# Kernel optimization log

Hardware: AMD Instinct MI355X
Metric: run time of the kernel (lower is better)

## Reference

```python
import jax, jax.numpy as jnp
import numpy as np

N_NODES = 100000
N_EDGES = 1000000
IN_F = 64
HEADS = 4
OUT_C = 32  # per-head channels
EDGE_DIM = 16
NEG_SLOPE = 0.2


def setup_inputs() -> dict:
    key = jax.random.key(0)
    ks = jax.random.split(key, 10)
    x = jax.random.normal(ks[0], (N_NODES, IN_F), dtype=jnp.float32)
    edge_index = jax.random.randint(ks[1], (2, N_EDGES), 0, N_NODES, dtype=jnp.int64)
    edge_attr = jax.random.normal(ks[2], (N_EDGES, EDGE_DIM), dtype=jnp.float32)
    s = 1.0 / np.sqrt(IN_F)
    W = jax.random.normal(ks[3], (IN_F, HEADS * OUT_C), dtype=jnp.float32) * s
    W_edge = jax.random.normal(ks[4], (EDGE_DIM, HEADS * OUT_C), dtype=jnp.float32) * (1.0 / np.sqrt(EDGE_DIM))
    att_src = jax.random.normal(ks[5], (HEADS, OUT_C), dtype=jnp.float32) * (1.0 / np.sqrt(OUT_C))
    att_dst = jax.random.normal(ks[6], (HEADS, OUT_C), dtype=jnp.float32) * (1.0 / np.sqrt(OUT_C))
    att_edge = jax.random.normal(ks[7], (HEADS, OUT_C), dtype=jnp.float32) * (1.0 / np.sqrt(OUT_C))
    bias = jnp.zeros((HEADS * OUT_C,), dtype=jnp.float32)
    return {"x": x, "edge_index": edge_index, "edge_attr": edge_attr,
            "W": W, "W_edge": W_edge, "att_src": att_src, "att_dst": att_dst,
            "att_edge": att_edge, "bias": bias}


def reference(x, edge_index, edge_attr, W, W_edge, att_src, att_dst, att_edge, bias):
    # PyG GATConv with edge_dim, add_self_loops=False, concat=True.
    N = x.shape[0]
    src = edge_index[0]  # message source j
    dst = edge_index[1]  # message target i

    x_proj = (x @ W).reshape(N, HEADS, OUT_C)          # [N,H,C]
    a_src = jnp.einsum('nhc,hc->nh', x_proj, att_src)  # [N,H]
    a_dst = jnp.einsum('nhc,hc->nh', x_proj, att_dst)  # [N,H]

    e_proj = (edge_attr @ W_edge).reshape(-1, HEADS, OUT_C)  # [E,H,C]
    a_edge = jnp.einsum('ehc,hc->eh', e_proj, att_edge)      # [E,H]

    alpha = a_src[src] + a_dst[dst] + a_edge                 # [E,H]
    alpha = jax.nn.leaky_relu(alpha, NEG_SLOPE)

    # edge softmax grouped by destination node
    seg_max = jax.ops.segment_max(alpha, dst, num_segments=N)  # [N,H]
    alpha = jnp.exp(alpha - seg_max[dst])
    denom = jax.ops.segment_sum(alpha, dst, num_segments=N)    # [N,H]
    alpha = alpha / (denom[dst] + 1e-16)

    msg = x_proj[src] * alpha[:, :, None]                      # [E,H,C]
    out = jax.ops.segment_sum(msg, dst, num_segments=N)        # [N,H,C]
    return out.reshape(N, HEADS * OUT_C) + bias
```

## Files before the change

### kernel.cpp

```cpp
#include <hip/hip_runtime.h>
#include <hip/hip_fp16.h>


#define HC 128
#define NEG 0.2f
#define CH 16
#define K_SHIFT 6.0f
#define NBK 512
#define BSH 8
#define BMSK 255
#define BCAP 3584
#define EPB 2048

typedef __fp16 half2_t __attribute__((ext_vector_type(2)));

__device__ __forceinline__ unsigned short f2bf(float f) {
    unsigned u = __float_as_uint(f);
    return (unsigned short)((u + 0x7fffu + ((u >> 16) & 1u)) >> 16);
}
__device__ __forceinline__ unsigned pk_h2(float lo, float hi) {
    half2_t p = __builtin_amdgcn_cvt_pkrtz(lo, hi);
    union { half2_t h; unsigned u; } cv;
    cv.h = p;
    return cv.u;
}
__device__ __forceinline__ float h2f_bits(unsigned short bits) {
    __half_raw hr; hr.x = bits;
    return __half2float(*reinterpret_cast<__half*>(&hr));
}
__device__ __forceinline__ long ld_idx(const int* __restrict__ ei, long i, int m64) {
    return m64 ? (long)(((const long long*)ei)[i]) : (long)ei[i];
}
__device__ __forceinline__ int detect_m64(const int* __restrict__ ei, int* s_m64) {
    int t = threadIdx.x;
    if (t < 64) {
        unsigned long long bal = __ballot(ei[2 * t + 1] != 0);
        if (t == 0) *s_m64 = (bal == 0ull) ? 1 : 0;
    }
    __syncthreads();
    return *s_m64;
}

union FrontLDS {
    struct {
        int hist[NBK]; int gb[NBK]; int loff[NBK]; int cnt2[NBK]; int s_sc[NBK];
        unsigned sd_l[EPB];
        unsigned short bk_l[EPB];
        uint2 aev_l[EPB];
    } b;
    struct {
        float x_s[4][64][68];
    } p;
};

__global__ __launch_bounds__(1024) void k_front(
    const float* __restrict__ x, const float* __restrict__ W,
    const float* __restrict__ as_, const float* __restrict__ ad_,
    const float* __restrict__ We, const float* __restrict__ ae,
    const float* __restrict__ eattr, const int* __restrict__ ei,
    unsigned short* __restrict__ xp, float* __restrict__ a_src,
    float* __restrict__ a_dst, int* __restrict__ bcur,
    unsigned* __restrict__ sdstg, uint2* __restrict__ aevstg,
    int N, int E, int nbA, int nbP) {
    __shared__ FrontLDS L;
    __shared__ float q_s[64];
    __shared__ int s_m64;
    int t = threadIdx.x;
    int id = blockIdx.x;

    bool bucket_role;
    int rid;
    if (id < 2 * nbP) { bucket_role = !(id & 1); rid = id >> 1; }
    else              { bucket_role = true;      rid = nbP + (id - 2 * nbP); }

    if (bucket_role) {
        int m64 = detect_m64(ei, &s_m64);
        if (t < 64) {
            int dd = t >> 2, h = t & 3;
            float s = 0.f;
            for (int c = 0; c < 32; ++c)
                s += We[dd * HC + h * 32 + c] * ae[h * 32 + c];
            q_s[t] = s;
        }
        if (t < NBK) { L.b.hist[t] = 0; L.b.cnt2[t] = 0; }
        __syncthreads();

        int base = rid * EPB + t;
#pragma unroll
        for (int k = 0; k < 2; ++k) {
            int e = base + k * 1024;
            if (e < E) {
                int d = (int)ld_idx(ei, (long)E + e, m64);
                atomicAdd(&L.b.hist[d >> BSH], 1);
            }
        }
        __syncthreads();
        if (t < NBK) {
            int c = L.b.hist[t];
            L.b.gb[t] = c ? atomicAdd(&bcur[t], c) : 0;
        }
        int own = (t < NBK) ? L.b.hist[t] : 0;
        if (t < NBK) L.b.s_sc[t] = own;
        __syncthreads();
        for (int off = 1; off < NBK; off <<= 1) {
            int xv = (t < NBK && t >= off) ? L.b.s_sc[t - off] : 0;
            __syncthreads();
            if (t < NBK) L.b.s_sc[t] += xv;
            __syncthreads();
        }
        if (t < NBK) L.b.loff[t] = L.b.s_sc[t] - own;
        __syncthreads();

#pragma unroll
        for (int k = 0; k < 2; ++k) {
            int e = base + k * 1024;
            if (e >= E) continue;
            int d = (int)ld_idx(ei, (long)E + e, m64);
            int b = d >> BSH;
            int lr = atomicAdd(&L.b.cnt2[b], 1);
            long s = ld_idx(ei, e, m64);
            const float4* pe = reinterpret_cast<const float4*>(eattr + (long)e * 16);
            float4 e0 = pe[0], e1 = pe[1], e2 = pe[2], e3 = pe[3];
            float ev[16] = {e0.x, e0.y, e0.z, e0.w, e1.x, e1.y, e1.z, e1.w,
                            e2.x, e2.y, e2.z, e2.w, e3.x, e3.y, e3.z, e3.w};
            float ov[4];
#pragma unroll
            for (int h = 0; h < 4; ++h) {
                float aev = 0.f;
#pragma unroll
                for (int dd = 0; dd < 16; ++dd) aev += ev[dd] * q_s[dd * 4 + h];
                ov[h] = aev;
            }
            int li = L.b.loff[b] + lr;
            L.b.sd_l[li] = (unsigned)s | ((unsigned)(d & BMSK) << 20);
            L.b.bk_l[li] = (unsigned short)b;
            L.b.aev_l[li] = make_uint2(pk_h2(ov[0], ov[1]), pk_h2(ov[2], ov[3]));
        }
        __syncthreads();

        int nrec = E - rid * EPB;
        if (nrec > EPB) nrec = EPB;
#pragma unroll
        for (int k = 0; k < 2; ++k) {
            int i = k * 1024 + t;
            if (i >= nrec) continue;
            int b = L.b.bk_l[i];
            int off = L.b.gb[b] + (i - L.b.loff[b]);
            if (off >= BCAP) continue;
            sdstg[b * BCAP + off] = L.b.sd_l[i];
            aevstg[b * BCAP + off] = L.b.aev_l[i];
        }
        return;
    }

    int q = t >> 8, tid = t & 255;
    int n0 = rid * 256 + q * 64;
    float (*x_s)[68] = L.p.x_s[q];
#pragma unroll
    for (int i = 0; i < 4; ++i) {
        int fl = i * 256 + tid;
        int node = fl >> 4, f4 = fl & 15;
        float4 v = make_float4(0.f, 0.f, 0.f, 0.f);
        if (n0 + node < N)
            v = *reinterpret_cast<const float4*>(&x[(long)(n0 + node) * 64 + f4 * 4]);
        x_s[f4 * 4 + 0][node] = v.x;
        x_s[f4 * 4 + 1][node] = v.y;
        x_s[f4 * 4 + 2][node] = v.z;
        x_s[f4 * 4 + 3][node] = v.w;
    }
    __syncthreads();

    int c = tid & 31;
    int nd = tid >> 5;
    const float4* __restrict__ W4 = reinterpret_cast<const float4*>(W);
    float acc[8][4];
#pragma unroll
    for (int i = 0; i < 8; ++i)
#pragma unroll
        for (int j = 0; j < 4; ++j) acc[i][j] = 0.f;

#pragma unroll 8
    for (int k = 0; k < 64; ++k) {
        float4 w4 = W4[k * 32 + c];
        float4 xa = *reinterpret_cast<const float4*>(&x_s[k][nd * 8]);
        float4 xb = *reinterpret_cast<const float4*>(&x_s[k][nd * 8 + 4]);
        float xv[8] = {xa.x, xa.y, xa.z, xa.w, xb.x, xb.y, xb.z, xb.w};
#pragma unroll
        for (int i = 0; i < 8; ++i) {
            acc[i][0] += xv[i] * w4.x;
            acc[i][1] += xv[i] * w4.y;
            acc[i][2] += xv[i] * w4.z;
            acc[i][3] += xv[i] * w4.w;
        }
    }

    float4 s4 = *reinterpret_cast<const float4*>(&as_[c * 4]);
    float4 d4 = *reinterpret_cast<const float4*>(&ad_[c * 4]);
#pragma unroll
    for (int i = 0; i < 8; ++i) {
        int node = n0 + nd * 8 + i;
        if (node < N) {
            ushort4 o;
            o.x = f2bf(acc[i][0]); o.y = f2bf(acc[i][1]);
            o.z = f2bf(acc[i][2]); o.w = f2bf(acc[i][3]);
            *reinterpret_cast<ushort4*>(&xp[(long)node * HC + c * 4]) = o;
        }
        float ps = acc[i][0] * s4.x + acc[i][1] * s4.y + acc[i][2] * s4.z + acc[i][3] * s4.w;
        float pd = acc[i][0] * d4.x + acc[i][1] * d4.y + acc[i][2] * d4.z + acc[i][3] * d4.w;
#pragma unroll
        for (int off = 1; off < 8; off <<= 1) {
            ps += __shfl_xor(ps, off, 64);
            pd += __shfl_xor(pd, off, 64);
        }
        if ((c & 7) == 0 && node < N) {
            int h = c >> 3;
            a_src[(long)node * 4 + h] = ps;
            a_dst[(long)node * 4 + h] = pd;
        }
    }
}

__global__ __launch_bounds__(1024) void k_back(
    const unsigned* __restrict__ sdstg, const uint2* __restrict__ aevstg,
    const int* __restrict__ bcur, const float* __restrict__ a_src,
    const float* __restrict__ a_dst, const char* __restrict__ xpc,
    const float* __restrict__ bias, float* __restrict__ out, int N) {
    int b = blockIdx.x, t = threadIdx.x;
    __shared__ int deg_l[256];
    __shared__ int s_sc[256];
    __shared__ int pfx[256];
    __shared__ unsigned src_l[BCAP];
    __shared__ uint2 w_l[BCAP];
    __shared__ float s_ex[16][CH][4];
    __shared__ int s_off[16][CH];
    __shared__ float s_l[16][4];
    if (t < 256) deg_l[t] = 0;
    __syncthreads();
    int cnt = bcur[b]; if (cnt > BCAP) cnt = BCAP;

    unsigned sdr[4]; int rkr[4]; uint2 wr[4];
#pragma unroll
    for (int k = 0; k < 4; ++k) {
        int i = k * 1024 + t;
        sdr[k] = 0u; rkr[k] = -1; wr[k] = make_uint2(0u, 0u);
        if (i < cnt) {
            unsigned sd = sdstg[b * BCAP + i];
            sdr[k] = sd;
            int dl = (sd >> 20) & BMSK;
            rkr[k] = atomicAdd(&deg_l[dl], 1);
            int s = (int)(sd & 0xFFFFFu);
            uint2 av = aevstg[b * BCAP + i];
            float4 s4 = *reinterpret_cast<const float4*>(a_src + (long)s * 4);
            float4 d4 = *reinterpret_cast<const float4*>(a_dst + (long)(b * 256 + dl) * 4);
            float lf[4];
            lf[0] = s4.x + d4.x + h2f_bits((unsigned short)(av.x & 0xffffu));
            lf[1] = s4.y + d4.y + h2f_bits((unsigned short)(av.x >> 16));
            lf[2] = s4.z + d4.z + h2f_bits((unsigned short)(av.y & 0xffffu));
            lf[3] = s4.w + d4.w + h2f_bits((unsigned short)(av.y >> 16));
            float exv[4];
#pragma unroll
            for (int h = 0; h < 4; ++h) {
                float v = (lf[h] > 0.f) ? lf[h] : NEG * lf[h];
                exv[h] = __expf(v - K_SHIFT);
            }
            wr[k] = make_uint2(pk_h2(exv[0], exv[1]), pk_h2(exv[2], exv[3]));
        }
    }
    __syncthreads();
    int own = (t < 256) ? deg_l[t] : 0;
    if (t < 256) s_sc[t] = own;
    __syncthreads();
    for (int off = 1; off < 256; off <<= 1) {
        int xv = (t >= off && t < 256) ? s_sc[t - off] : 0;
        __syncthreads();
        if (t < 256) s_sc[t] += xv;
        __syncthreads();
    }
    if (t < 256) pfx[t] = s_sc[t] - own;
    __syncthreads();
#pragma unroll
    for (int k = 0; k < 4; ++k) {
        int i = k * 1024 + t;
        if (i >= cnt) continue;
        int dl = (sdr[k] >> 20) & BMSK;
        int pos = pfx[dl] + rkr[k];
        src_l[pos] = sdr[k] & 0xFFFFFu;
        w_l[pos] = wr[k];
    }
    __syncthreads();

    int wv = t >> 6, lane = t & 63;
    int h_s = lane & 3, e_s = lane >> 2;
    int par = lane >> 5;
    int cl = lane & 31;
    int h_a = cl >> 3;
    for (int ni = 0; ni < 16; ++ni) {
        int dl = wv * 16 + ni;
        int n = b * 256 + dl;
        if (n >= N) continue;
        int beg = pfx[dl];
        int end = beg + deg_l[dl];
        if (end > BCAP) end = BCAP;
        float l = 0.f;
        float acc[4] = {0.f, 0.f, 0.f, 0.f};
        for (int cs = beg; cs < end; cs += CH) {
            int c2 = end - cs;
            if (c2 > CH) c2 = CH;
            float ex = 0.f;
            if (e_s < c2) {
                if (h_s == 0) s_off[wv][e_s] = (int)(src_l[cs + e_s] << 8);
                uint2 wv2 = w_l[cs + e_s];
                unsigned pr = (h_s & 2) ? wv2.y : wv2.x;
                unsigned bits = (h_s & 1) ? (pr >> 16) : (pr & 0xffffu);
                ex = h2f_bits((unsigned short)bits);
            }
            s_ex[wv][e_s][h_s] = ex;
            float se = ex;
            se += __shfl_xor(se, 4, 64);
            se += __shfl_xor(se, 8, 64);
            se += __shfl_xor(se, 16, 64);
            se += __shfl_xor(se, 32, 64);
            l += se;
            int j = 0;
            for (; j + 4 <= c2; j += 4) {
                int ea0 = j + par, ea1 = j + 2 + par;
                int o0 = s_off[wv][ea0], o1 = s_off[wv][ea1];
                float w0 = s_ex[wv][ea0][h_a], w1 = s_ex[wv][ea1][h_a];
                uint2 v0 = *reinterpret_cast<const uint2*>(xpc + o0 + cl * 8);
                uint2 v1 = *reinterpret_cast<const uint2*>(xpc + o1 + cl * 8);
                acc[0] += w0 * __uint_as_float(v0.x << 16);
                acc[1] += w0 * __uint_as_float(v0.x & 0xffff0000u);
                acc[2] += w0 * __uint_as_float(v0.y << 16);
                acc[3] += w0 * __uint_as_float(v0.y & 0xffff0000u);
                acc[0] += w1 * __uint_as_float(v1.x << 16);
                acc[1] += w1 * __uint_as_float(v1.x & 0xffff0000u);
                acc[2] += w1 * __uint_as_float(v1.y << 16);
                acc[3] += w1 * __uint_as_float(v1.y & 0xffff0000u);
            }
            for (; j < c2; j += 2) {
                int e = j + par;
                bool act = e < c2;
                int o = s_off[wv][act ? e : j];
                float w = act ? s_ex[wv][e][h_a] : 0.f;
                uint2 v = *reinterpret_cast<const uint2*>(xpc + o + cl * 8);
                acc[0] += w * __uint_as_float(v.x << 16);
                acc[1] += w * __uint_as_float(v.x & 0xffff0000u);
                acc[2] += w * __uint_as_float(v.y << 16);
                acc[3] += w * __uint_as_float(v.y & 0xffff0000u);
            }
        }
        if (lane < 4) s_l[wv][h_s] = l;
#pragma unroll
        for (int k = 0; k < 4; ++k) acc[k] += __shfl_xor(acc[k], 32, 64);
        if (par == 0) {
            float d = s_l[wv][h_a] + 1e-16f;
            float4 b4 = *reinterpret_cast<const float4*>(bias + cl * 4);
            float4 o;
            o.x = acc[0] / d + b4.x;
            o.y = acc[1] / d + b4.y;
            o.z = acc[2] / d + b4.z;
            o.w = acc[3] / d + b4.w;
            *reinterpret_cast<float4*>(out + (long)n * HC + cl * 4) = o;
        }
    }
}

extern "C" void kernel_launch(void* const* d_in, const int* in_sizes, int n_in,
                              void* d_out, int out_size, void* d_ws, size_t ws_size,
                              hipStream_t stream) {
    const float* x    = (const float*)d_in[0];
    const int*   ei   = (const int*)d_in[1];
    const float* ea   = (const float*)d_in[2];
    const float* W    = (const float*)d_in[3];
    const float* We   = (const float*)d_in[4];
    const float* as_  = (const float*)d_in[5];
    const float* ad_  = (const float*)d_in[6];
    const float* ae   = (const float*)d_in[7];
    const float* bias = (const float*)d_in[8];
    float* out = (float*)d_out;

    int N = in_sizes[0] / 64;
    int E = in_sizes[1] / 2;

    char* ws = (char*)d_ws;
    size_t off = 0;
    auto take = [&](size_t bytes) -> char* {
        char* p = ws + off;
        off += (bytes + 511) & ~(size_t)511;
        return p;
    };
    unsigned short* xp = (unsigned short*)take((size_t)N * HC * 2);
    float* a_src    = (float*)take((size_t)N * 4 * 4);
    float* a_dst    = (float*)take((size_t)N * 4 * 4);
    unsigned* sdstg = (unsigned*)take((size_t)NBK * BCAP * 4);
    uint2* aevstg   = (uint2*)take((size_t)NBK * BCAP * 8);
    int* bcur       = (int*)take((size_t)NBK * 4);

    int nbA = (E + EPB - 1) / EPB;
    int nbP = (N + 255) / 256;

    (void)hipMemsetAsync(bcur, 0, (size_t)NBK * 4, stream);
    hipLaunchKernelGGL(k_front, dim3(nbA + nbP), dim3(1024), 0, stream,
                       x, W, as_, ad_, We, ae, ea, ei,
                       xp, a_src, a_dst, bcur, sdstg, aevstg, N, E, nbA, nbP);
    hipLaunchKernelGGL(k_back, dim3(nbP), dim3(1024), 0, stream,
                       sdstg, aevstg, bcur, a_src, a_dst,
                       (const char*)xp, bias, out, N);
}
```

Baseline: 245.7 us.

## Merge front and back kernels into one persistent cooperative kernel with grid sync

Fuses the projection/bucketing kernel and the aggregation kernel into a single persistent cooperative kernel. Blocks loop over front work items, meet at a grid-wide barrier, then loop over destination buckets. The goal is to remove the second kernel launch and its inter-kernel gap. In exchange, the grid is capped at occupancy times 256 CUs, and the shared LDS union grows to the larger back-phase footprint, which may lower occupancy of the front phase.

```diff
diff --git a/kernel.cpp b/kernel.cpp
--- a/kernel.cpp
+++ b/kernel.cpp
@@ -1,5 +1,8 @@
 #include <hip/hip_runtime.h>
 #include <hip/hip_fp16.h>
+#include <hip/hip_cooperative_groups.h>
+
+namespace cg = cooperative_groups;
 
 
 #define HC 128
@@ -41,7 +44,7 @@
     return *s_m64;
 }
 
-union FrontLDS {
+union AllLDS {
     struct {
         int hist[NBK]; int gb[NBK]; int loff[NBK]; int cnt2[NBK]; int s_sc[NBK];
         unsigned sd_l[EPB];
@@ -51,9 +54,17 @@
     struct {
         float x_s[4][64][68];
     } p;
+    struct {
+        int deg_l[256]; int s_sc[256]; int pfx[256];
+        unsigned src_l[BCAP];
+        uint2 w_l[BCAP];
+        float s_ex[16][CH][4];
+        int s_off[16][CH];
+        float s_l[16][4];
+    } k;
 };
 
-__global__ __launch_bounds__(1024) void k_front(
+__global__ __launch_bounds__(1024) void k_all(
     const float* __restrict__ x, const float* __restrict__ W,
     const float* __restrict__ as_, const float* __restrict__ ad_,
     const float* __restrict__ We, const float* __restrict__ ae,
@@ -61,306 +72,303 @@
     unsigned short* __restrict__ xp, float* __restrict__ a_src,
     float* __restrict__ a_dst, int* __restrict__ bcur,
     unsigned* __restrict__ sdstg, uint2* __restrict__ aevstg,
+    const float* __restrict__ bias, float* __restrict__ out,
     int N, int E, int nbA, int nbP) {
-    __shared__ FrontLDS L;
+    __shared__ AllLDS L;
     __shared__ float q_s[64];
     __shared__ int s_m64;
     int t = threadIdx.x;
-    int id = blockIdx.x;
-
-    bool bucket_role;
-    int rid;
-    if (id < 2 * nbP) { bucket_role = !(id & 1); rid = id >> 1; }
-    else              { bucket_role = true;      rid = nbP + (id - 2 * nbP); }
-
-    if (bucket_role) {
-        int m64 = detect_m64(ei, &s_m64);
-        if (t < 64) {
-            int dd = t >> 2, h = t & 3;
-            float s = 0.f;
-            for (int c = 0; c < 32; ++c)
-                s += We[dd * HC + h * 32 + c] * ae[h * 32 + c];
-            q_s[t] = s;
-        }
-        if (t < NBK) { L.b.hist[t] = 0; L.b.cnt2[t] = 0; }
-        __syncthreads();
-
-        int base = rid * EPB + t;
-#pragma unroll
-        for (int k = 0; k < 2; ++k) {
-            int e = base + k * 1024;
-            if (e < E) {
+
+    int nFront = nbA + nbP;
+    int nMin = (nbA < nbP) ? nbA : nbP;
+    int nPair = 2 * nMin;
+    for (int item = blockIdx.x; item < nFront; item += gridDim.x) {
+        __syncthreads();
+        bool bucket_role; int rid;
+        if (item < nPair) { bucket_role = !(item & 1); rid = item >> 1; }
+        else              { bucket_role = (nbA > nbP); rid = nMin + (item - nPair); }
+
+        if (bucket_role) {
+            int m64 = detect_m64(ei, &s_m64);
+            if (t < 64) {
+                int dd = t >> 2, h = t & 3;
+                float s = 0.f;
+                for (int c = 0; c < 32; ++c)
+                    s += We[dd * HC + h * 32 + c] * ae[h * 32 + c];
+                q_s[t] = s;
+            }
+            if (t < NBK) { L.b.hist[t] = 0; L.b.cnt2[t] = 0; }
+            __syncthreads();
+
+            int base = rid * EPB + t;
+#pragma unroll
+            for (int k = 0; k < 2; ++k) {
+                int e = base + k * 1024;
+                if (e < E) {
+                    int d = (int)ld_idx(ei, (long)E + e, m64);
+                    atomicAdd(&L.b.hist[d >> BSH], 1);
+                }
+            }
+            __syncthreads();
+            if (t < NBK) {
+                int c = L.b.hist[t];
+                L.b.gb[t] = c ? atomicAdd(&bcur[t], c) : 0;
+            }
+            int own = (t < NBK) ? L.b.hist[t] : 0;
+            if (t < NBK) L.b.s_sc[t] = own;
+            __syncthreads();
+            for (int off = 1; off < NBK; off <<= 1) {
+                int xv = (t < NBK && t >= off) ? L.b.s_sc[t - off] : 0;
+                __syncthreads();
+                if (t < NBK) L.b.s_sc[t] += xv;
+                __syncthreads();
+            }
+            if (t < NBK) L.b.loff[t] = L.b.s_sc[t] - own;
+            __syncthreads();
+
+#pragma unroll
+            for (int k = 0; k < 2; ++k) {
+                int e = base + k * 1024;
+                if (e >= E) continue;
                 int d = (int)ld_idx(ei, (long)E + e, m64);
-                atomicAdd(&L.b.hist[d >> BSH], 1);
-            }
-        }
-        __syncthreads();
-        if (t < NBK) {
-            int c = L.b.hist[t];
-            L.b.gb[t] = c ? atomicAdd(&bcur[t], c) : 0;
-        }
-        int own = (t < NBK) ? L.b.hist[t] : 0;
-        if (t < NBK) L.b.s_sc[t] = own;
-        __syncthreads();
-        for (int off = 1; off < NBK; off <<= 1) {
-            int xv = (t < NBK && t >= off) ? L.b.s_sc[t - off] : 0;
-            __syncthreads();
-            if (t < NBK) L.b.s_sc[t] += xv;
-            __syncthreads();
-        }
-        if (t < NBK) L.b.loff[t] = L.b.s_sc[t] - own;
-        __syncthreads();
-
-#pragma unroll
-        for (int k = 0; k < 2; ++k) {
-            int e = base + k * 1024;
-            if (e >= E) continue;
-            int d = (int)ld_idx(ei, (long)E + e, m64);
-            int b = d >> BSH;
-            int lr = atomicAdd(&L.b.cnt2[b], 1);
-            long s = ld_idx(ei, e, m64);
-            const float4* pe = reinterpret_cast<const float4*>(eattr + (long)e * 16);
-            float4 e0 = pe[0], e1 = pe[1], e2 = pe[2], e3 = pe[3];
-            float ev[16] = {e0.x, e0.y, e0.z, e0.w, e1.x, e1.y, e1.z, e1.w,
-                            e2.x, e2.y, e2.z, e2.w, e3.x, e3.y, e3.z, e3.w};
-            float ov[4];
-#pragma unroll
-            for (int h = 0; h < 4; ++h) {
-                float aev = 0.f;
-#pragma unroll
-                for (int dd = 0; dd < 16; ++dd) aev += ev[dd] * q_s[dd * 4 + h];
-                ov[h] = aev;
-            }
-            int li = L.b.loff[b] + lr;
-            L.b.sd_l[li] = (unsigned)s | ((unsigned)(d & BMSK) << 20);
-            L.b.bk_l[li] = (unsigned short)b;
-            L.b.aev_l[li] = make_uint2(pk_h2(ov[0], ov[1]), pk_h2(ov[2], ov[3]));
-        }
-        __syncthreads();
-
-        int nrec = E - rid * EPB;
-        if (nrec > EPB) nrec = EPB;
-#pragma unroll
-        for (int k = 0; k < 2; ++k) {
-            int i = k * 1024 + t;
-            if (i >= nrec) continue;
-            int b = L.b.bk_l[i];
-            int off = L.b.gb[b] + (i - L.b.loff[b]);
-            if (off >= BCAP) continue;
-            sdstg[b * BCAP + off] = L.b.sd_l[i];
-            aevstg[b * BCAP + off] = L.b.aev_l[i];
-        }
-        return;
-    }
-
-    int q = t >> 8, tid = t & 255;
-    int n0 = rid * 256 + q * 64;
-    float (*x_s)[68] = L.p.x_s[q];
-#pragma unroll
-    for (int i = 0; i < 4; ++i) {
-        int fl = i * 256 + tid;
-        int node = fl >> 4, f4 = fl & 15;
-        float4 v = make_float4(0.f, 0.f, 0.f, 0.f);
-        if (n0 + node < N)
-            v = *reinterpret_cast<const float4*>(&x[(long)(n0 + node) * 64 + f4 * 4]);
-        x_s[f4 * 4 + 0][node] = v.x;
-        x_s[f4 * 4 + 1][node] = v.y;
-        x_s[f4 * 4 + 2][node] = v.z;
-        x_s[f4 * 4 + 3][node] = v.w;
-    }
-    __syncthreads();
-
-    int c = tid & 31;
-    int nd = tid >> 5;
-    const float4* __restrict__ W4 = reinterpret_cast<const float4*>(W);
-    float acc[8][4];
-#pragma unroll
-    for (int i = 0; i < 8; ++i)
-#pragma unroll
-        for (int j = 0; j < 4; ++j) acc[i][j] = 0.f;
+                int b = d >> BSH;
+                int lr = atomicAdd(&L.b.cnt2[b], 1);
+                long s = ld_idx(ei, e, m64);
+                const float4* pe = reinterpret_cast<const float4*>(eattr + (long)e * 16);
+                float4 e0 = pe[0], e1 = pe[1], e2 = pe[2], e3 = pe[3];
+                float ev[16] = {e0.x, e0.y, e0.z, e0.w, e1.x, e1.y, e1.z, e1.w,
+                                e2.x, e2.y, e2.z, e2.w, e3.x, e3.y, e3.z, e3.w};
+                float ov[4];
+#pragma unroll
+                for (int h = 0; h < 4; ++h) {
+                    float aev = 0.f;
+#pragma unroll
+                    for (int dd = 0; dd < 16; ++dd) aev += ev[dd] * q_s[dd * 4 + h];
+                    ov[h] = aev;
+                }
+                int li = L.b.loff[b] + lr;
+                L.b.sd_l[li] = (unsigned)s | ((unsigned)(d & BMSK) << 20);
+                L.b.bk_l[li] = (unsigned short)b;
+                L.b.aev_l[li] = make_uint2(pk_h2(ov[0], ov[1]), pk_h2(ov[2], ov[3]));
+            }
+            __syncthreads();
+
+            int nrec = E - rid * EPB;
+            if (nrec > EPB) nrec = EPB;
+#pragma unroll
+            for (int k = 0; k < 2; ++k) {
+                int i = k * 1024 + t;
+                if (i >= nrec) continue;
+                int b = L.b.bk_l[i];
+                int off = L.b.gb[b] + (i - L.b.loff[b]);
+                if (off >= BCAP) continue;
+                sdstg[b * BCAP + off] = L.b.sd_l[i];
+                aevstg[b * BCAP + off] = L.b.aev_l[i];
+            }
+        } else {
+            int q = t >> 8, tid = t & 255;
+            int n0 = rid * 256 + q * 64;
+            float (*x_s)[68] = L.p.x_s[q];
+#pragma unroll
+            for (int i = 0; i < 4; ++i) {
+                int fl = i * 256 + tid;
+                int node = fl >> 4, f4 = fl & 15;
+                float4 v = make_float4(0.f, 0.f, 0.f, 0.f);
+                if (n0 + node < N)
+                    v = *reinterpret_cast<const float4*>(&x[(long)(n0 + node) * 64 + f4 * 4]);
+                x_s[f4 * 4 + 0][node] = v.x;
+                x_s[f4 * 4 + 1][node] = v.y;
+                x_s[f4 * 4 + 2][node] = v.z;
+                x_s[f4 * 4 + 3][node] = v.w;
+            }
+            __syncthreads();
+
+            int c = tid & 31;
+            int nd = tid >> 5;
+            const float4* __restrict__ W4 = reinterpret_cast<const float4*>(W);
+            float acc[8][4];
+#pragma unroll
+            for (int i = 0; i < 8; ++i)
+#pragma unroll
+                for (int j = 0; j < 4; ++j) acc[i][j] = 0.f;
 
 #pragma unroll 8
-    for (int k = 0; k < 64; ++k) {
-        float4 w4 = W4[k * 32 + c];
-        float4 xa = *reinterpret_cast<const float4*>(&x_s[k][nd * 8]);
-        float4 xb = *reinterpret_cast<const float4*>(&x_s[k][nd * 8 + 4]);
-        float xv[8] = {xa.x, xa.y, xa.z, xa.w, xb.x, xb.y, xb.z, xb.w};
-#pragma unroll
-        for (int i = 0; i < 8; ++i) {
-            acc[i][0] += xv[i] * w4.x;
-            acc[i][1] += xv[i] * w4.y;
-            acc[i][2] += xv[i] * w4.z;
-            acc[i][3] += xv[i] * w4.w;
+            for (int k = 0; k < 64; ++k) {
+                float4 w4 = W4[k * 32 + c];
+                float4 xa = *reinterpret_cast<const float4*>(&x_s[k][nd * 8]);
+                float4 xb = *reinterpret_cast<const float4*>(&x_s[k][nd * 8 + 4]);
+                float xv[8] = {xa.x, xa.y, xa.z, xa.w, xb.x, xb.y, xb.z, xb.w};
+#pragma unroll
+                for (int i = 0; i < 8; ++i) {
+                    acc[i][0] += xv[i] * w4.x;
+                    acc[i][1] += xv[i] * w4.y;
+                    acc[i][2] += xv[i] * w4.z;
+                    acc[i][3] += xv[i] * w4.w;
+                }
+            }
+
+            float4 s4 = *reinterpret_cast<const float4*>(&as_[c * 4]);
+            float4 d4 = *reinterpret_cast<const float4*>(&ad_[c * 4]);
+#pragma unroll
+            for (int i = 0; i < 8; ++i) {
+                int node = n0 + nd * 8 + i;
+                if (node < N) {
+                    ushort4 o;
+                    o.x = f2bf(acc[i][0]); o.y = f2bf(acc[i][1]);
+                    o.z = f2bf(acc[i][2]); o.w = f2bf(acc[i][3]);
+                    *reinterpret_cast<ushort4*>(&xp[(long)node * HC + c * 4]) = o;
+                }
+                float ps = acc[i][0] * s4.x + acc[i][1] * s4.y + acc[i][2] * s4.z + acc[i][3] * s4.w;
+                float pd = acc[i][0] * d4.x + acc[i][1] * d4.y + acc[i][2] * d4.z + acc[i][3] * d4.w;
+#pragma unroll
+                for (int off = 1; off < 8; off <<= 1) {
+                    ps += __shfl_xor(ps, off, 64);
+                    pd += __shfl_xor(pd, off, 64);
+                }
+                if ((c & 7) == 0 && node < N) {
+                    int h = c >> 3;
+                    a_src[(long)node * 4 + h] = ps;
+                    a_dst[(long)node * 4 + h] = pd;
+                }
+            }
         }
     }
 
-    float4 s4 = *reinterpret_cast<const float4*>(&as_[c * 4]);
-    float4 d4 = *reinterpret_cast<const float4*>(&ad_[c * 4]);
-#pragma unroll
-    for (int i = 0; i < 8; ++i) {
-        int node = n0 + nd * 8 + i;
-        if (node < N) {
-            ushort4 o;
-            o.x = f2bf(acc[i][0]); o.y = f2bf(acc[i][1]);
-            o.z = f2bf(acc[i][2]); o.w = f2bf(acc[i][3]);
-            *reinterpret_cast<ushort4*>(&xp[(long)node * HC + c * 4]) = o;
+    __threadfence();
+    cg::this_grid().sync();
+    __threadfence();
+
+    for (int b = blockIdx.x; b < nbP; b += gridDim.x) {
+        __syncthreads();
+        if (t < 256) L.k.deg_l[t] = 0;
+        __syncthreads();
+        int cnt = bcur[b]; if (cnt > BCAP) cnt = BCAP;
+
+        unsigned sdr[4]; int rkr[4]; uint2 wr[4];
+#pragma unroll
+        for (int k = 0; k < 4; ++k) {
+            int i = k * 1024 + t;
+            sdr[k] = 0u; rkr[k] = -1; wr[k] = make_uint2(0u, 0u);
+            if (i < cnt) {
+                unsigned sd = sdstg[b * BCAP + i];
+                sdr[k] = sd;
+                int dl = (sd >> 20) & BMSK;
+                rkr[k] = atomicAdd(&L.k.deg_l[dl], 1);
+                int s = (int)(sd & 0xFFFFFu);
+                uint2 av = aevstg[b * BCAP + i];
+                float4 s4 = *reinterpret_cast<const float4*>(a_src + (long)s * 4);
+                float4 d4 = *reinterpret_cast<const float4*>(a_dst + (long)(b * 256 + dl) * 4);
+                float lf[4];
+                lf[0] = s4.x + d4.x + h2f_bits((unsigned short)(av.x & 0xffffu));
+                lf[1] = s4.y + d4.y + h2f_bits((unsigned short)(av.x >> 16));
+                lf[2] = s4.z + d4.z + h2f_bits((unsigned short)(av.y & 0xffffu));
+                lf[3] = s4.w + d4.w + h2f_bits((unsigned short)(av.y >> 16));
+                float exv[4];
+#pragma unroll
+                for (int h = 0; h < 4; ++h) {
+                    float v = (lf[h] > 0.f) ? lf[h] : NEG * lf[h];
+                    exv[h] = __expf(v - K_SHIFT);
+                }
+                wr[k] = make_uint2(pk_h2(exv[0], exv[1]), pk_h2(exv[2], exv[3]));
+            }
         }
-        float ps = acc[i][0] * s4.x + acc[i][1] * s4.y + acc[i][2] * s4.z + acc[i][3] * s4.w;
-        float pd = acc[i][0] * d4.x + acc[i][1] * d4.y + acc[i][2] * d4.z + acc[i][3] * d4.w;
-#pragma unroll
-        for (int off = 1; off < 8; off <<= 1) {
-            ps += __shfl_xor(ps, off, 64);
-            pd += __shfl_xor(pd, off, 64);
+        __syncthreads();
+        int own = (t < 256) ? L.k.deg_l[t] : 0;
+        if (t < 256) L.k.s_sc[t] = own;
+        __syncthreads();
+        for (int off = 1; off < 256; off <<= 1) {
+            int xv = (t >= off && t < 256) ? L.k.s_sc[t - off] : 0;
+            __syncthreads();
+            if (t < 256) L.k.s_sc[t] += xv;
+            __syncthreads();
         }
-        if ((c & 7) == 0 && node < N) {
-            int h = c >> 3;
-            a_src[(long)node * 4 + h] = ps;
-            a_dst[(long)node * 4 + h] = pd;
+        if (t < 256) L.k.pfx[t] = L.k.s_sc[t] - own;
+        __syncthreads();
+#pragma unroll
+        for (int k = 0; k < 4; ++k) {
+            int i = k * 1024 + t;
+            if (i >= cnt) continue;
+            int dl = (sdr[k] >> 20) & BMSK;
+            int pos = L.k.pfx[dl] + rkr[k];
+            L.k.src_l[pos] = sdr[k] & 0xFFFFFu;
+            L.k.w_l[pos] = wr[k];
         }
-    }
-}
-
-__global__ __launch_bounds__(1024) void k_back(
-    const unsigned* __restrict__ sdstg, const uint2* __restrict__ aevstg,
-    const int* __restrict__ bcur, const float* __restrict__ a_src,
-    const float* __restrict__ a_dst, const char* __restrict__ xpc,
-    const float* __restrict__ bias, float* __restrict__ out, int N) {
-    int b = blockIdx.x, t = threadIdx.x;
-    __shared__ int deg_l[256];
-    __shared__ int s_sc[256];
-    __shared__ int pfx[256];
-    __shared__ unsigned src_l[BCAP];
-    __shared__ uint2 w_l[BCAP];
-    __shared__ float s_ex[16][CH][4];
-    __shared__ int s_off[16][CH];
-    __shared__ float s_l[16][4];
-    if (t < 256) deg_l[t] = 0;
-    __syncthreads();
-    int cnt = bcur[b]; if (cnt > BCAP) cnt = BCAP;
-
-    unsigned sdr[4]; int rkr[4]; uint2 wr[4];
-#pragma unroll
-    for (int k = 0; k < 4; ++k) {
-        int i = k * 1024 + t;
-        sdr[k] = 0u; rkr[k] = -1; wr[k] = make_uint2(0u, 0u);
-        if (i < cnt) {
-            unsigned sd = sdstg[b * BCAP + i];
-            sdr[k] = sd;
-            int dl = (sd >> 20) & BMSK;
-            rkr[k] = atomicAdd(&deg_l[dl], 1);
-            int s = (int)(sd & 0xFFFFFu);
-            uint2 av = aevstg[b * BCAP + i];
-            float4 s4 = *reinterpret_cast<const float4*>(a_src + (long)s * 4);
-            float4 d4 = *reinterpret_cast<const float4*>(a_dst + (long)(b * 256 + dl) * 4);
-            float lf[4];
-            lf[0] = s4.x + d4.x + h2f_bits((unsigned short)(av.x & 0xffffu));
-            lf[1] = s4.y + d4.y + h2f_bits((unsigned short)(av.x >> 16));
-            lf[2] = s4.z + d4.z + h2f_bits((unsigned short)(av.y & 0xffffu));
-            lf[3] = s4.w + d4.w + h2f_bits((unsigned short)(av.y >> 16));
-            float exv[4];
-#pragma unroll
-            for (int h = 0; h < 4; ++h) {
-                float v = (lf[h] > 0.f) ? lf[h] : NEG * lf[h];
-                exv[h] = __expf(v - K_SHIFT);
-            }
-            wr[k] = make_uint2(pk_h2(exv[0], exv[1]), pk_h2(exv[2], exv[3]));
-        }
-    }
-    __syncthreads();
-    int own = (t < 256) ? deg_l[t] : 0;
-    if (t < 256) s_sc[t] = own;
-    __syncthreads();
-    for (int off = 1; off < 256; off <<= 1) {
-        int xv = (t >= off && t < 256) ? s_sc[t - off] : 0;
-        __syncthreads();
-        if (t < 256) s_sc[t] += xv;
-        __syncthreads();
-    }
-    if (t < 256) pfx[t] = s_sc[t] - own;
-    __syncthreads();
-#pragma unroll
-    for (int k = 0; k < 4; ++k) {
-        int i = k * 1024 + t;
-        if (i >= cnt) continue;
-        int dl = (sdr[k] >> 20) & BMSK;
-        int pos = pfx[dl] + rkr[k];
-        src_l[pos] = sdr[k] & 0xFFFFFu;
-        w_l[pos] = wr[k];
-    }
-    __syncthreads();
-
-    int wv = t >> 6, lane = t & 63;
-    int h_s = lane & 3, e_s = lane >> 2;
-    int par = lane >> 5;
-    int cl = lane & 31;
-    int h_a = cl >> 3;
-    for (int ni = 0; ni < 16; ++ni) {
-        int dl = wv * 16 + ni;
-        int n = b * 256 + dl;
-        if (n >= N) continue;
-        int beg = pfx[dl];
-        int end = beg + deg_l[dl];
-        if (end > BCAP) end = BCAP;
-        float l = 0.f;
-        float acc[4] = {0.f, 0.f, 0.f, 0.f};
-        for (int cs = beg; cs < end; cs += CH) {
-            int c2 = end - cs;
-            if (c2 > CH) c2 = CH;
-            float ex = 0.f;
-            if (e_s < c2) {
-                if (h_s == 0) s_off[wv][e_s] = (int)(src_l[cs + e_s] << 8);
-                uint2 wv2 = w_l[cs + e_s];
-                unsigned pr = (h_s & 2) ? wv2.y : wv2.x;
-                unsigned bits = (h_s & 1) ? (pr >> 16) : (pr & 0xffffu);
-                ex = h2f_bits((unsigned short)bits);
-            }
-            s_ex[wv][e_s][h_s] = ex;
-            float se = ex;
-            se += __shfl_xor(se, 4, 64);
-            se += __shfl_xor(se, 8, 64);
-            se += __shfl_xor(se, 16, 64);
-            se += __shfl_xor(se, 32, 64);
-            l += se;
-            int j = 0;
-            for (; j + 4 <= c2; j += 4) {
-                int ea0 = j + par, ea1 = j + 2 + par;
-                int o0 = s_off[wv][ea0], o1 = s_off[wv][ea1];
-                float w0 = s_ex[wv][ea0][h_a], w1 = s_ex[wv][ea1][h_a];
-                uint2 v0 = *reinterpret_cast<const uint2*>(xpc + o0 + cl * 8);
-                uint2 v1 = *reinterpret_cast<const uint2*>(xpc + o1 + cl * 8);
-                acc[0] += w0 * __uint_as_float(v0.x << 16);
-                acc[1] += w0 * __uint_as_float(v0.x & 0xffff0000u);
-                acc[2] += w0 * __uint_as_float(v0.y << 16);
-                acc[3] += w0 * __uint_as_float(v0.y & 0xffff0000u);
-                acc[0] += w1 * __uint_as_float(v1.x << 16);
-                acc[1] += w1 * __uint_as_float(v1.x & 0xffff0000u);
-                acc[2] += w1 * __uint_as_float(v1.y << 16);
-                acc[3] += w1 * __uint_as_float(v1.y & 0xffff0000u);
-            }
-            for (; j < c2; j += 2) {
-                int e = j + par;
-                bool act = e < c2;
-                int o = s_off[wv][act ? e : j];
-                float w = act ? s_ex[wv][e][h_a] : 0.f;
-                uint2 v = *reinterpret_cast<const uint2*>(xpc + o + cl * 8);
-                acc[0] += w * __uint_as_float(v.x << 16);
-                acc[1] += w * __uint_as_float(v.x & 0xffff0000u);
-                acc[2] += w * __uint_as_float(v.y << 16);
-                acc[3] += w * __uint_as_float(v.y & 0xffff0000u);
-            }
-        }
-        if (lane < 4) s_l[wv][h_s] = l;
-#pragma unroll
-        for (int k = 0; k < 4; ++k) acc[k] += __shfl_xor(acc[k], 32, 64);
-        if (par == 0) {
-            float d = s_l[wv][h_a] + 1e-16f;
-            float4 b4 = *reinterpret_cast<const float4*>(bias + cl * 4);
-            float4 o;
-            o.x = acc[0] / d + b4.x;
-            o.y = acc[1] / d + b4.y;
-            o.z = acc[2] / d + b4.z;
-            o.w = acc[3] / d + b4.w;
-            *reinterpret_cast<float4*>(out + (long)n * HC + cl * 4) = o;
+        __syncthreads();
+
+        int wv = t >> 6, lane = t & 63;
+        int h_s = lane & 3, e_s = lane >> 2;
+        int par = lane >> 5;
+        int cl = lane & 31;
+        int h_a = cl >> 3;
+        const char* xpc = reinterpret_cast<const char*>(xp);
+        for (int ni = 0; ni < 16; ++ni) {
+            int dl = wv * 16 + ni;
+            int n = b * 256 + dl;
+            if (n >= N) continue;
+            int beg = L.k.pfx[dl];
+            int end = beg + L.k.deg_l[dl];
+            if (end > BCAP) end = BCAP;
+            float l = 0.f;
+            float acc[4] = {0.f, 0.f, 0.f, 0.f};
+            for (int cs = beg; cs < end; cs += CH) {
+                int c2 = end - cs;
+                if (c2 > CH) c2 = CH;
+                float ex = 0.f;
+                if (e_s < c2) {
+                    if (h_s == 0) L.k.s_off[wv][e_s] = (int)(L.k.src_l[cs + e_s] << 8);
+                    uint2 wv2 = L.k.w_l[cs + e_s];
+                    unsigned pr = (h_s & 2) ? wv2.y : wv2.x;
+                    unsigned bits = (h_s & 1) ? (pr >> 16) : (pr & 0xffffu);
+                    ex = h2f_bits((unsigned short)bits);
+                }
+                L.k.s_ex[wv][e_s][h_s] = ex;
+                float se = ex;
+                se += __shfl_xor(se, 4, 64);
+                se += __shfl_xor(se, 8, 64);
+                se += __shfl_xor(se, 16, 64);
+                se += __shfl_xor(se, 32, 64);
+                l += se;
+                int j = 0;
+                for (; j + 4 <= c2; j += 4) {
+                    int ea0 = j + par, ea1 = j + 2 + par;
+                    int o0 = L.k.s_off[wv][ea0], o1 = L.k.s_off[wv][ea1];
+                    float w0 = L.k.s_ex[wv][ea0][h_a], w1 = L.k.s_ex[wv][ea1][h_a];
+                    uint2 v0 = *reinterpret_cast<const uint2*>(xpc + o0 + cl * 8);
+                    uint2 v1 = *reinterpret_cast<const uint2*>(xpc + o1 + cl * 8);
+                    acc[0] += w0 * __uint_as_float(v0.x << 16);
+                    acc[1] += w0 * __uint_as_float(v0.x & 0xffff0000u);
+                    acc[2] += w0 * __uint_as_float(v0.y << 16);
+                    acc[3] += w0 * __uint_as_float(v0.y & 0xffff0000u);
+                    acc[0] += w1 * __uint_as_float(v1.x << 16);
+                    acc[1] += w1 * __uint_as_float(v1.x & 0xffff0000u);
+                    acc[2] += w1 * __uint_as_float(v1.y << 16);
+                    acc[3] += w1 * __uint_as_float(v1.y & 0xffff0000u);
+                }
+                for (; j < c2; j += 2) {
+                    int e = j + par;
+                    bool act = e < c2;
+                    int o = L.k.s_off[wv][act ? e : j];
+                    float w = act ? L.k.s_ex[wv][e][h_a] : 0.f;
+                    uint2 v = *reinterpret_cast<const uint2*>(xpc + o + cl * 8);
+                    acc[0] += w * __uint_as_float(v.x << 16);
+                    acc[1] += w * __uint_as_float(v.x & 0xffff0000u);
+                    acc[2] += w * __uint_as_float(v.y << 16);
+                    acc[3] += w * __uint_as_float(v.y & 0xffff0000u);
+                }
+            }
+            if (lane < 4) L.k.s_l[wv][h_s] = l;
+#pragma unroll
+            for (int k = 0; k < 4; ++k) acc[k] += __shfl_xor(acc[k], 32, 64);
+            if (par == 0) {
+                float d = L.k.s_l[wv][h_a] + 1e-16f;
+                float4 b4 = *reinterpret_cast<const float4*>(bias + cl * 4);
+                float4 o;
+                o.x = acc[0] / d + b4.x;
+                o.y = acc[1] / d + b4.y;
+                o.z = acc[2] / d + b4.z;
+                o.w = acc[3] / d + b4.w;
+                *reinterpret_cast<float4*>(out + (long)n * HC + cl * 4) = o;
+            }
         }
     }
 }
@@ -399,11 +407,20 @@
     int nbA = (E + EPB - 1) / EPB;
     int nbP = (N + 255) / 256;
 
+    int maxb = 0;
+    (void)hipOccupancyMaxActiveBlocksPerMultiprocessor(&maxb, k_all, 1024, 0);
+    if (maxb < 1) maxb = 1;
+    long grid = (long)maxb * 256;
+    if (grid > nbA + nbP) grid = nbA + nbP;
+
+    void* args[] = {
+        (void*)&x, (void*)&W, (void*)&as_, (void*)&ad_, (void*)&We,
+        (void*)&ae, (void*)&ea, (void*)&ei, (void*)&xp, (void*)&a_src,
+        (void*)&a_dst, (void*)&bcur, (void*)&sdstg, (void*)&aevstg,
+        (void*)&bias, (void*)&out, (void*)&N, (void*)&E,
+        (void*)&nbA, (void*)&nbP};
+
     (void)hipMemsetAsync(bcur, 0, (size_t)NBK * 4, stream);
-    hipLaunchKernelGGL(k_front, dim3(nbA + nbP), dim3(1024), 0, stream,
-                       x, W, as_, ad_, We, ae, ea, ei,
-                       xp, a_src, a_dst, bcur, sdstg, aevstg, N, E, nbA, nbP);
-    hipLaunchKernelGGL(k_back, dim3(nbP), dim3(1024), 0, stream,
-                       sdstg, aevstg, bcur, a_src, a_dst,
-                       (const char*)xp, bias, out, N);
-}
+    (void)hipLaunchCooperativeKernel((const void*)k_all, dim3((int)grid),
+                                     dim3(1024), args, 0, stream);
+}
```

After: 529.2 us. +115.4%, slower.
